# Kernel optimization log

Measured on AMD Instinct MI355X. Metric: run time of the kernel, lower is better.

The kernel has to match this reference:

```python
import math
import jax, jax.numpy as jnp
import numpy as np

HIDDEN = 2048
HEAD_DIM = 128
NUM_HEADS = 32
NUM_KV_HEADS = 8
GROUP = NUM_HEADS // NUM_KV_HEADS
B, S = 1, 2048


def setup_inputs() -> dict:
    key = jax.random.key(0)
    ks = jax.random.split(key, 9)
    scale_in = 1.0 / math.sqrt(HIDDEN)
    scale_o = 1.0 / math.sqrt(NUM_HEADS * HEAD_DIM)
    x = jax.random.normal(ks[0], (B, S, HIDDEN), dtype=jnp.float32)
    # causal mask (1,1,S,S), int32; masked positions are 0
    mask = jnp.tril(jnp.ones((S, S), dtype=jnp.int32))[None, None]
    wq = jax.random.uniform(ks[1], (HIDDEN, NUM_HEADS * HEAD_DIM), jnp.float32, -scale_in, scale_in)
    bq = jax.random.uniform(ks[2], (NUM_HEADS * HEAD_DIM,), jnp.float32, -scale_in, scale_in)
    wk = jax.random.uniform(ks[3], (HIDDEN, NUM_KV_HEADS * HEAD_DIM), jnp.float32, -scale_in, scale_in)
    bk = jax.random.uniform(ks[4], (NUM_KV_HEADS * HEAD_DIM,), jnp.float32, -scale_in, scale_in)
    wv = jax.random.uniform(ks[5], (HIDDEN, NUM_KV_HEADS * HEAD_DIM), jnp.float32, -scale_in, scale_in)
    bv = jax.random.uniform(ks[6], (NUM_KV_HEADS * HEAD_DIM,), jnp.float32, -scale_in, scale_in)
    wo = jax.random.uniform(ks[7], (NUM_HEADS * HEAD_DIM, HIDDEN), jnp.float32, -scale_o, scale_o)
    bo = jax.random.uniform(ks[8], (HIDDEN,), jnp.float32, -scale_o, scale_o)
    return {"x": x, "mask": mask, "wq": wq, "bq": bq, "wk": wk, "bk": bk,
            "wv": wv, "bv": bv, "wo": wo, "bo": bo}


def reference(x, mask, wq, bq, wk, bk, wv, bv, wo, bo):
    Bb, Ss, _ = x.shape
    inv_sqrt_d = 1.0 / math.sqrt(HEAD_DIM)
    # projections
    q = (x @ wq + bq).reshape(Bb, Ss, NUM_KV_HEADS, GROUP, HEAD_DIM)  # grouped query heads
    k = (x @ wk + bk).reshape(Bb, Ss, NUM_KV_HEADS, HEAD_DIM)
    v = (x @ wv + bv).reshape(Bb, Ss, NUM_KV_HEADS, HEAD_DIM)
    # repeat_interleave(group, dim=2) on k/v == broadcasting each kv head over its
    # GROUP consecutive query heads; einsum avoids the physical KV blow-up.
    scores = jnp.einsum('bqhgd,bshd->bhgqs', q, k) * inv_sqrt_d  # (B, Hkv, G, S, S)
    m = mask[:, :, None]  # (1,1,1,S,S) broadcasts over (Hkv, G)
    scores = jnp.where(m == 0, -jnp.inf, scores)
    attn = jax.nn.softmax(scores, axis=-1)
    out = jnp.einsum('bhgqs,bshd->bqhgd', attn, v).reshape(Bb, Ss, NUM_HEADS * HEAD_DIM)
    return out @ wo + bo
```

## Files before the change

kernel.cpp:

```cpp
#include <hip/hip_runtime.h>

#define HIDDEN 2048
#define S_LEN  2048
#define NH     32
#define NKV    8
#define HD     128
#define QKVN   6144
#define OD     4096

typedef float  f32x4   __attribute__((ext_vector_type(4)));
typedef float  f32x16  __attribute__((ext_vector_type(16)));
typedef __bf16 bf16x8  __attribute__((ext_vector_type(8)));
typedef __bf16 bf16x4  __attribute__((ext_vector_type(4)));
typedef unsigned int u32;

static __device__ __forceinline__ f32x4 mfma16(bf16x8 a, bf16x8 b, f32x4 c) {
  return __builtin_amdgcn_mfma_f32_16x16x32_bf16(a, b, c, 0, 0, 0);
}
static __device__ __forceinline__ f32x16 mfma32(bf16x8 a, bf16x8 b, f32x16 c) {
  return __builtin_amdgcn_mfma_f32_32x32x16_bf16(a, b, c, 0, 0, 0);
}
static __device__ __forceinline__ void gload_lds16(const void* g, void* l) {
  __builtin_amdgcn_global_load_lds(
      (__attribute__((address_space(1))) void*)(g),
      (__attribute__((address_space(3))) void*)(l), 16, 0, 0);
}
static __device__ __forceinline__ u32 pk_bf16(float lo, float hi) {
  u32 r;
  asm("v_cvt_pk_bf16_f32 %0, %1, %2" : "=v"(r) : "v"(lo), "v"(hi));
  return r;
}

__global__ __launch_bounds__(256) void k_cvt(const float* __restrict__ in,
                                             __bf16* __restrict__ out, int n) {
  int i = (blockIdx.x * 256 + threadIdx.x) * 4;
  if (i >= n) return;
  float4 v = *reinterpret_cast<const float4*>(in + i);
  bf16x4 o = {(__bf16)v.x, (__bf16)v.y, (__bf16)v.z, (__bf16)v.w};
  *reinterpret_cast<bf16x4*>(out + i) = o;
}

__global__ __launch_bounds__(256) void k_transpose_cvt(const float* __restrict__ src,
                                                       __bf16* __restrict__ dst,
                                                       int K, int N) {
  __shared__ float tile[32][33];
  int tx = threadIdx.x & 31, ty = threadIdx.x >> 5;
  int n0 = blockIdx.x * 32, k0 = blockIdx.y * 32;
#pragma unroll
  for (int r = 0; r < 4; r++) {
    int k = ty + r * 8;
    tile[k][tx] = src[(size_t)(k0 + k) * N + n0 + tx];
  }
  __syncthreads();
#pragma unroll
  for (int r = 0; r < 4; r++) {
    int n = ty + r * 8;
    dst[(size_t)(n0 + n) * K + k0 + tx] = (__bf16)tile[tx][n];
  }
}

__global__ void k_bias_concat(const float* __restrict__ bq, const float* __restrict__ bk,
                              const float* __restrict__ bv, float* __restrict__ out) {
  int i = blockIdx.x * 256 + threadIdx.x;
  if (i >= QKVN) return;
  out[i] = (i < 4096) ? bq[i] : (i < 5120 ? bk[i - 4096] : bv[i - 5120]);
}

__global__ __launch_bounds__(256) void k_vtrans(const __bf16* __restrict__ qkv,
                                                __bf16* __restrict__ vt) {
  __shared__ __bf16 tile[32][33];
  int tx = threadIdx.x & 31, ty = threadIdx.x >> 5;
  int s0 = blockIdx.x * 32, d0 = blockIdx.y * 32, kv = blockIdx.z;
#pragma unroll
  for (int r = 0; r < 4; r++) {
    int s = ty + r * 8;
    tile[s][tx] = qkv[(size_t)(s0 + s) * QKVN + 5120 + kv * HD + d0 + tx];
  }
  __syncthreads();
#pragma unroll
  for (int r = 0; r < 4; r++) {
    int d = ty + r * 8;
    vt[(size_t)(kv * HD + d0 + d) * S_LEN + s0 + tx] = tile[tx][d];
  }
}

__global__ __launch_bounds__(512, 2) void k_gemm8(const __bf16* __restrict__ A,
                                                  const __bf16* __restrict__ BT,
                                                  const float* __restrict__ bias,
                                                  __bf16* __restrict__ C,
                                                  int M, int N, int K,
                                                  float oscale, int scale_cols) {
  __shared__ __bf16 Al[2][2][8192];
  __shared__ __bf16 Bl[2][2][8192];
  const int tid = threadIdx.x, lane = tid & 63, w = tid >> 6;
  const int l15 = lane & 15, lhi = lane >> 4;
  const int wr = w >> 2, wc = w & 3;
  const int mt = blockIdx.x & 7, nt = blockIdx.x >> 3;
  const int m0 = mt * 256, n0 = nt * 256;
  const int NKT = K >> 6;
  const __bf16* Ab = A + (size_t)m0 * K;
  const __bf16* Bb = BT + (size_t)n0 * K;

  f32x4 acc[8][4];
#pragma unroll
  for (int i = 0; i < 8; i++)
#pragma unroll
    for (int j = 0; j < 4; j++)
#pragma unroll
      for (int e = 0; e < 4; e++) acc[i][j][e] = 0.f;

#define SGH(dstA, srcB, buf, kh, ktile)                                           \
  do {                                                                            \
    _Pragma("unroll") for (int it = 0; it < 2; ++it) {                            \
      int c = it * 512 + tid;                                                     \
      int row = c >> 2, slot = c & 3;                                             \
      int scol = ((slot * 16) ^ (((row >> 1) & 3) << 4)) >> 1;                    \
      gload_lds16(srcB + (size_t)row * K + (ktile) * 64 + (kh) * 32 + scol,       \
                  &dstA[buf][kh][c * 8]);                                         \
    }                                                                             \
  } while (0)

#define RD_A(cb, kk)                                                              \
  do {                                                                            \
    _Pragma("unroll") for (int i = 0; i < 8; ++i) {                               \
      int row = wr * 128 + i * 16 + l15;                                          \
      af[i] = *(const bf16x8*)(&Al[cb][kk][row * 32 +                             \
                (((lhi * 16) ^ (((row >> 1) & 3) << 4)) >> 1)]);                  \
    }                                                                             \
  } while (0)

#define RD_B4(cb, kk)                                                             \
  do {                                                                            \
    _Pragma("unroll") for (int j = 0; j < 4; ++j) {                               \
      int row = wc * 64 + j * 16 + l15;                                           \
      bfr[j] = *(const bf16x8*)(&Bl[cb][kk][row * 32 +                            \
                (((lhi * 16) ^ (((row >> 1) & 3) << 4)) >> 1)]);                  \
    }                                                                             \
  } while (0)

#define MFMA32X                                                                   \
  do {                                                                            \
    __builtin_amdgcn_s_setprio(1);                                                \
    _Pragma("unroll") for (int i = 0; i < 8; ++i) {                               \
      _Pragma("unroll") for (int j = 0; j < 4; ++j) {                             \
        acc[i][j] = mfma16(af[i], bfr[j], acc[i][j]);                             \
      }                                                                           \
    }                                                                             \
    __builtin_amdgcn_s_setprio(0);                                                \
  } while (0)

  SGH(Al, Ab, 0, 0, 0);
  SGH(Bl, Bb, 0, 0, 0);
  SGH(Al, Ab, 0, 1, 0);
  SGH(Bl, Bb, 0, 1, 0);
  asm volatile("s_waitcnt vmcnt(4)" ::: "memory");
  __builtin_amdgcn_s_barrier();
  __builtin_amdgcn_sched_barrier(0);

  for (int kt = 0; kt < NKT; ++kt) {
    const int cb = kt & 1, pb = cb ^ 1;
    const bool pf = (kt + 1 < NKT);
    bf16x8 af[8], bfr[4];

    RD_A(cb, 0);
    RD_B4(cb, 0);
    if (pf) { SGH(Al, Ab, pb, 0, kt + 1); SGH(Bl, Bb, pb, 0, kt + 1); }
    __builtin_amdgcn_s_barrier();
    asm volatile("s_waitcnt lgkmcnt(0)" ::: "memory");
    MFMA32X;
    if (pf) {
      asm volatile("s_waitcnt vmcnt(4)" ::: "memory");
    } else {
      asm volatile("s_waitcnt vmcnt(0)" ::: "memory");
    }
    __builtin_amdgcn_s_barrier();
    __builtin_amdgcn_sched_barrier(0);

    RD_A(cb, 1);
    RD_B4(cb, 1);
    if (pf) { SGH(Al, Ab, pb, 1, kt + 1); SGH(Bl, Bb, pb, 1, kt + 1); }
    __builtin_amdgcn_s_barrier();
    asm volatile("s_waitcnt lgkmcnt(0)" ::: "memory");
    MFMA32X;
    if (pf) {
      asm volatile("s_waitcnt vmcnt(4)" ::: "memory");
    }
    __builtin_amdgcn_s_barrier();
    __builtin_amdgcn_sched_barrier(0);
  }
#undef SGH
#undef RD_A
#undef RD_B4
#undef MFMA32X

#pragma unroll
  for (int j = 0; j < 4; j++) {
    int col = n0 + wc * 64 + j * 16 + l15;
    float bv = bias[col];
    float sc = (col < scale_cols) ? oscale : 1.0f;
#pragma unroll
    for (int i = 0; i < 8; i++) {
      int r0 = m0 + wr * 128 + i * 16 + lhi * 4;
#pragma unroll
      for (int rr = 0; rr < 4; rr++) {
        C[(size_t)(r0 + rr) * N + col] = (__bf16)((acc[i][j][rr] + bv) * sc);
      }
    }
  }
}

__global__ __launch_bounds__(256) void k_gemm_part(const __bf16* __restrict__ A,
                                                   const __bf16* __restrict__ BT,
                                                   float* __restrict__ Cpart,
                                                   int M, int N, int K, int KC) {
  __shared__ __bf16 Al[128 * 64];
  __shared__ __bf16 Bl[128 * 64];
  const int tid = threadIdx.x;
  const int lane = tid & 63;
  const int w = tid >> 6;
  const int m0 = blockIdx.y * 128;
  const int n0 = blockIdx.x * 128;
  const int kbeg = blockIdx.z * KC;
  const int wm = (w >> 1) * 64;
  const int wn = (w & 1) * 64;
  const int l15 = lane & 15, lhi = lane >> 4;

  f32x4 acc[4][4];
#pragma unroll
  for (int i = 0; i < 4; i++)
#pragma unroll
    for (int j = 0; j < 4; j++)
#pragma unroll
      for (int e = 0; e < 4; e++) acc[i][j][e] = 0.f;

  for (int kt = kbeg; kt < kbeg + KC; kt += 64) {
#pragma unroll
    for (int it = 0; it < 4; it++) {
      int idx = it * 256 + tid;
      int row = idx >> 3, slot = idx & 7;
      int scol = ((slot * 16) ^ ((row & 7) << 4)) >> 1;
      gload_lds16(A + (size_t)(m0 + row) * K + kt + scol, &Al[idx * 8]);
      gload_lds16(BT + (size_t)(n0 + row) * K + kt + scol, &Bl[idx * 8]);
    }
    __syncthreads();
#pragma unroll
    for (int kk = 0; kk < 2; kk++) {
      bf16x8 af[4], bfr[4];
#pragma unroll
      for (int i = 0; i < 4; i++) {
        int ra = wm + i * 16 + l15;
        int ba = (kk * 64 + lhi * 16) ^ ((ra & 7) << 4);
        af[i] = *(const bf16x8*)((const char*)Al + ra * 128 + ba);
        int rb = wn + i * 16 + l15;
        int bb = (kk * 64 + lhi * 16) ^ ((rb & 7) << 4);
        bfr[i] = *(const bf16x8*)((const char*)Bl + rb * 128 + bb);
      }
#pragma unroll
      for (int i = 0; i < 4; i++)
#pragma unroll
        for (int j = 0; j < 4; j++) acc[i][j] = mfma16(af[i], bfr[j], acc[i][j]);
    }
    __syncthreads();
  }
  float* C = Cpart + (size_t)blockIdx.z * M * N;
#pragma unroll
  for (int j = 0; j < 4; j++) {
    int col = n0 + wn + j * 16 + l15;
#pragma unroll
    for (int i = 0; i < 4; i++) {
      int r0 = m0 + wm + i * 16 + lhi * 4;
#pragma unroll
      for (int rr = 0; rr < 4; rr++) {
        C[(size_t)(r0 + rr) * N + col] = acc[i][j][rr];
      }
    }
  }
}

__global__ __launch_bounds__(256) void k_ocombine(const float* __restrict__ a,
                                                  const float* __restrict__ b,
                                                  const float* __restrict__ bias,
                                                  float* __restrict__ out) {
  int i = (blockIdx.x * 256 + threadIdx.x) * 4;
  f32x4 va = *(const f32x4*)(a + i);
  f32x4 vb = *(const f32x4*)(b + i);
  f32x4 vbias = *(const f32x4*)(bias + (i & (HIDDEN - 1)));
  f32x4 r = va + vb + vbias;
  *(f32x4*)(out + i) = r;
}

__global__ __launch_bounds__(256, 2) void k_attn(const __bf16* __restrict__ qkv,
                                                 const __bf16* __restrict__ vt,
                                                 __bf16* __restrict__ o) {
  __shared__ __bf16 Kl[2][8192];
  __shared__ __bf16 Vl[2][8192];
  const int tid = threadIdx.x, lane = tid & 63, w = tid >> 6;
  const int l31 = lane & 31, h = lane >> 5;

  const int id = blockIdx.x;
  int tile, head;
  if (id < 256) { head = id >> 4; tile = id & 15; }
  else          { head = 16 + ((id - 256) >> 4); tile = 15 - (id & 15); }
  const int kvh = head >> 2;
  const int qbase = tile * 128 + w * 32;
  const int qg = qbase + l31;
  const int kdiag = (qbase + 31) >> 6;
  const int nkt = 2 * tile + 2;

  bf16x8 qf[8];
  {
    const __bf16* qrow = qkv + (size_t)qg * QKVN + head * HD;
#pragma unroll
    for (int dk = 0; dk < 8; dk++) qf[dk] = *(const bf16x8*)(qrow + dk * 16 + h * 8);
  }

  f32x16 acc[4];
#pragma unroll
  for (int dt = 0; dt < 4; dt++)
#pragma unroll
    for (int r = 0; r < 16; r++) acc[dt][r] = 0.f;
  float m = -INFINITY, lsum = 0.f;

#define STAGE(buf, ktile)                                                           \
  do {                                                                              \
    const int kk0 = (ktile) * 64;                                                   \
    _Pragma("unroll") for (int it = 0; it < 4; it++) {                              \
      int c = it * 256 + tid;                                                       \
      int key = c >> 4, slot = c & 15;                                              \
      int scol = ((slot * 16) ^ ((key & 15) << 4)) >> 1;                            \
      gload_lds16(qkv + (size_t)(kk0 + key) * QKVN + 4096 + kvh * HD + scol,        \
                  &Kl[buf][c * 8]);                                                 \
    }                                                                               \
    _Pragma("unroll") for (int it = 0; it < 4; it++) {                              \
      int c = it * 256 + tid;                                                       \
      int d = c >> 3, slot = c & 7;                                                 \
      int scol = ((slot * 16) ^ ((d & 7) << 4)) >> 1;                               \
      gload_lds16(vt + (size_t)(kvh * HD + d) * S_LEN + kk0 + scol,                 \
                  &Vl[buf][c * 8]);                                                 \
    }                                                                               \
  } while (0)

  STAGE(0, 0);
  __syncthreads();

  for (int kt = 0; kt < nkt; kt++) {
    const int cur = kt & 1;
    if (kt + 1 < nkt) STAGE(cur ^ 1, kt + 1);

    if (kt <= kdiag) {
      const char* Kb = (const char*)&Kl[cur][0];
      const char* Vb = (const char*)&Vl[cur][0];
      const int k0 = kt * 64;
      f32x16 sacc[2];
#pragma unroll
      for (int b = 0; b < 2; b++)
#pragma unroll
        for (int r = 0; r < 16; r++) sacc[b][r] = 0.f;
      __builtin_amdgcn_s_setprio(1);
#pragma unroll
      for (int dk = 0; dk < 8; dk++) {
        const int sA = ((2 * dk + h) ^ (l31 & 15)) * 16;
        bf16x8 kf0 = *(const bf16x8*)(Kb + l31 * 256 + sA);
        bf16x8 kf1 = *(const bf16x8*)(Kb + (32 + l31) * 256 + sA);
        sacc[0] = mfma32(kf0, qf[dk], sacc[0]);
        sacc[1] = mfma32(kf1, qf[dk], sacc[1]);
      }
      __builtin_amdgcn_s_setprio(0);
      float p[32];
#pragma unroll
      for (int b = 0; b < 2; b++)
#pragma unroll
        for (int r = 0; r < 16; r++) p[b * 16 + r] = sacc[b][r];
      if (kt == kdiag) {
#pragma unroll
        for (int b = 0; b < 2; b++)
#pragma unroll
          for (int r = 0; r < 16; r++) {
            int keyg = k0 + b * 32 + (r & 3) + 8 * (r >> 2) + 4 * h;
            if (keyg > qg) p[b * 16 + r] = -INFINITY;
          }
      }
      float t16[16], t8[8], t4[4];
#pragma unroll
      for (int i = 0; i < 16; i++) t16[i] = fmaxf(p[2 * i], p[2 * i + 1]);
#pragma unroll
      for (int i = 0; i < 8; i++) t8[i] = fmaxf(t16[2 * i], t16[2 * i + 1]);
#pragma unroll
      for (int i = 0; i < 4; i++) t4[i] = fmaxf(t8[2 * i], t8[2 * i + 1]);
      float pm = fmaxf(fmaxf(t4[0], t4[1]), fmaxf(t4[2], t4[3]));
      pm = fmaxf(pm, __shfl_xor(pm, 32));
      if (__any(pm - m > 8.f)) {
        float mn = fmaxf(m, pm);
        float corr = __expf(m - mn);
        m = mn;
        lsum *= corr;
#pragma unroll
        for (int dt = 0; dt < 4; dt++)
#pragma unroll
          for (int r = 0; r < 16; r++) acc[dt][r] *= corr;
      }
      float psum = 0.f;
#pragma unroll
      for (int i = 0; i < 32; i++) { p[i] = __expf(p[i] - m); psum += p[i]; }
      lsum += psum;
#pragma unroll
      for (int ks2 = 0; ks2 < 4; ks2++) {
        const int o8 = (ks2 >> 1) * 16 + (ks2 & 1) * 8;
        u32 W0 = pk_bf16(p[o8 + 0], p[o8 + 1]);
        u32 W1 = pk_bf16(p[o8 + 2], p[o8 + 3]);
        u32 W2 = pk_bf16(p[o8 + 4], p[o8 + 5]);
        u32 W3 = pk_bf16(p[o8 + 6], p[o8 + 7]);
        asm("v_permlane32_swap_b32 %0, %1" : "+v"(W0), "+v"(W2));
        asm("v_permlane32_swap_b32 %0, %1" : "+v"(W1), "+v"(W3));
        union { u32 wd[4]; bf16x8 v; } pu;
        pu.wd[0] = W0; pu.wd[1] = W1; pu.wd[2] = W2; pu.wd[3] = W3;
        __builtin_amdgcn_s_setprio(1);
#pragma unroll
        for (int dt = 0; dt < 4; dt++) {
          const int dr = dt * 32 + l31;
          const int sV = ((2 * ks2 + h) ^ (dr & 7)) * 16;
          bf16x8 vf = *(const bf16x8*)(Vb + dr * 128 + sV);
          acc[dt] = mfma32(vf, pu.v, acc[dt]);
        }
        __builtin_amdgcn_s_setprio(0);
      }
    }
    __syncthreads();
  }
#undef STAGE

  lsum += __shfl_xor(lsum, 32);
  const float inv = 1.f / lsum;
  __bf16* orow = o + (size_t)qg * OD + head * HD;
#pragma unroll
  for (int dt = 0; dt < 4; dt++)
#pragma unroll
    for (int rq = 0; rq < 4; rq++) {
      int d = dt * 32 + 8 * rq + 4 * h;
      bf16x4 ov = {(__bf16)(acc[dt][rq * 4 + 0] * inv), (__bf16)(acc[dt][rq * 4 + 1] * inv),
                   (__bf16)(acc[dt][rq * 4 + 2] * inv), (__bf16)(acc[dt][rq * 4 + 3] * inv)};
      *(bf16x4*)(orow + d) = ov;
    }
}

extern "C" void kernel_launch(void* const* d_in, const int* in_sizes, int n_in,
                              void* d_out, int out_size, void* d_ws, size_t ws_size,
                              hipStream_t stream) {
  const float* x  = (const float*)d_in[0];
  const float* wq = (const float*)d_in[2];
  const float* bq = (const float*)d_in[3];
  const float* wk = (const float*)d_in[4];
  const float* bk = (const float*)d_in[5];
  const float* wv = (const float*)d_in[6];
  const float* bv = (const float*)d_in[7];
  const float* wo = (const float*)d_in[8];
  const float* bo = (const float*)d_in[9];
  float* out = (float*)d_out;

  const size_t MB = 1024 * 1024;
  char* ws = (char*)d_ws;
  __bf16* xb    = (__bf16*)(ws);
  __bf16* wqkvT = (__bf16*)(ws + 8 * MB);
  __bf16* woT   = (__bf16*)(ws + 32 * MB);
  __bf16* qkvb  = (__bf16*)(ws + 48 * MB);
  __bf16* vtb   = (__bf16*)(ws + 72 * MB);
  __bf16* ob    = (__bf16*)(ws + 76 * MB);
  float*  bqkv  = (float*)(ws + 92 * MB);
  float*  Cpart = (float*)(ws);

  k_cvt<<<4096, 256, 0, stream>>>(x, xb, HIDDEN * S_LEN);
  k_transpose_cvt<<<dim3(128, 64), 256, 0, stream>>>(wq, wqkvT, HIDDEN, 4096);
  k_transpose_cvt<<<dim3(32, 64), 256, 0, stream>>>(wk, wqkvT + (size_t)4096 * HIDDEN, HIDDEN, 1024);
  k_transpose_cvt<<<dim3(32, 64), 256, 0, stream>>>(wv, wqkvT + (size_t)5120 * HIDDEN, HIDDEN, 1024);
  k_transpose_cvt<<<dim3(64, 128), 256, 0, stream>>>(wo, woT, 4096, HIDDEN);
  k_bias_concat<<<24, 256, 0, stream>>>(bq, bk, bv, bqkv);

  k_gemm8<<<192, 512, 0, stream>>>(xb, wqkvT, bqkv, qkvb, S_LEN, QKVN, HIDDEN,
                                   0.08838834764831845f, 4096);
  k_vtrans<<<dim3(S_LEN / 32, HD / 32, NKV), 256, 0, stream>>>(qkvb, vtb);
  k_attn<<<512, 256, 0, stream>>>(qkvb, vtb, ob);
  k_gemm_part<<<dim3(HIDDEN / 128, S_LEN / 128, 2), 256, 0, stream>>>(
      ob, woT, Cpart, S_LEN, HIDDEN, OD, OD / 2);
  k_ocombine<<<(S_LEN * HIDDEN) / 1024, 256, 0, stream>>>(
      Cpart, Cpart + (size_t)S_LEN * HIDDEN, bo, out);
}
```

Before: 224.6 us.

## Retile QKV GEMM to 128x192 tiles with 256 threads and XCD-aware block swizzle

The QKV projection GEMM moves from 192 blocks of 256x256 tiles with 512 threads to 512 blocks of 128x192 tiles with 256 threads. Each wave now covers all 128 rows and a 48-column slice, and the load and wait counts change to match. A block index swizzle groups tiles per XCD so neighbouring blocks share operands in cache. The aim is to fill all 256 CUs (192 blocks left many idle) at the cost of lower per-tile data reuse and more redundant global loads.

```diff
diff --git a/kernel.cpp b/kernel.cpp
--- a/kernel.cpp
+++ b/kernel.cpp
@@ -84,123 +84,121 @@
   }
 }
 
-__global__ __launch_bounds__(512, 2) void k_gemm8(const __bf16* __restrict__ A,
+__global__ __launch_bounds__(256, 2) void k_gemm8(const __bf16* __restrict__ A,
                                                   const __bf16* __restrict__ BT,
                                                   const float* __restrict__ bias,
                                                   __bf16* __restrict__ C,
                                                   int M, int N, int K,
                                                   float oscale, int scale_cols) {
-  __shared__ __bf16 Al[2][2][8192];
-  __shared__ __bf16 Bl[2][2][8192];
+  __shared__ __bf16 Al[2][2][4096];
+  __shared__ __bf16 Bl[2][2][6144];
   const int tid = threadIdx.x, lane = tid & 63, w = tid >> 6;
   const int l15 = lane & 15, lhi = lane >> 4;
-  const int wr = w >> 2, wc = w & 3;
-  const int mt = blockIdx.x & 7, nt = blockIdx.x >> 3;
-  const int m0 = mt * 256, n0 = nt * 256;
+  const int sw = ((blockIdx.x & 7) << 6) + (blockIdx.x >> 3);
+  const int mt = sw & 15, nt = sw >> 4;
+  const int m0 = mt * 128, n0 = nt * 192;
   const int NKT = K >> 6;
   const __bf16* Ab = A + (size_t)m0 * K;
   const __bf16* Bb = BT + (size_t)n0 * K;
 
-  f32x4 acc[8][4];
+  f32x4 acc[8][3];
 #pragma unroll
   for (int i = 0; i < 8; i++)
 #pragma unroll
-    for (int j = 0; j < 4; j++)
+    for (int j = 0; j < 3; j++)
 #pragma unroll
       for (int e = 0; e < 4; e++) acc[i][j][e] = 0.f;
 
-#define SGH(dstA, srcB, buf, kh, ktile)                                           \
+#define SGH(buf, kh, ktile)                                                       \
   do {                                                                            \
     _Pragma("unroll") for (int it = 0; it < 2; ++it) {                            \
-      int c = it * 512 + tid;                                                     \
+      int c = it * 256 + tid;                                                     \
       int row = c >> 2, slot = c & 3;                                             \
       int scol = ((slot * 16) ^ (((row >> 1) & 3) << 4)) >> 1;                    \
-      gload_lds16(srcB + (size_t)row * K + (ktile) * 64 + (kh) * 32 + scol,       \
-                  &dstA[buf][kh][c * 8]);                                         \
+      gload_lds16(Ab + (size_t)row * K + (ktile) * 64 + (kh) * 32 + scol,         \
+                  &Al[buf][kh][c * 8]);                                           \
+    }                                                                             \
+    _Pragma("unroll") for (int it = 0; it < 3; ++it) {                            \
+      int c = it * 256 + tid;                                                     \
+      int row = c >> 2, slot = c & 3;                                             \
+      int scol = ((slot * 16) ^ (((row >> 1) & 3) << 4)) >> 1;                    \
+      gload_lds16(Bb + (size_t)row * K + (ktile) * 64 + (kh) * 32 + scol,         \
+                  &Bl[buf][kh][c * 8]);                                           \
     }                                                                             \
   } while (0)
 
-#define RD_A(cb, kk)                                                              \
+#define RD_AB(cb, kk)                                                             \
   do {                                                                            \
     _Pragma("unroll") for (int i = 0; i < 8; ++i) {                               \
-      int row = wr * 128 + i * 16 + l15;                                          \
+      int row = i * 16 + l15;                                                     \
       af[i] = *(const bf16x8*)(&Al[cb][kk][row * 32 +                             \
                 (((lhi * 16) ^ (((row >> 1) & 3) << 4)) >> 1)]);                  \
     }                                                                             \
-  } while (0)
-
-#define RD_B4(cb, kk)                                                             \
-  do {                                                                            \
-    _Pragma("unroll") for (int j = 0; j < 4; ++j) {                               \
-      int row = wc * 64 + j * 16 + l15;                                           \
+    _Pragma("unroll") for (int j = 0; j < 3; ++j) {                               \
+      int row = w * 48 + j * 16 + l15;                                            \
       bfr[j] = *(const bf16x8*)(&Bl[cb][kk][row * 32 +                            \
                 (((lhi * 16) ^ (((row >> 1) & 3) << 4)) >> 1)]);                  \
     }                                                                             \
   } while (0)
 
-#define MFMA32X                                                                   \
+#define MFMA24X                                                                   \
   do {                                                                            \
     __builtin_amdgcn_s_setprio(1);                                                \
     _Pragma("unroll") for (int i = 0; i < 8; ++i) {                               \
-      _Pragma("unroll") for (int j = 0; j < 4; ++j) {                             \
+      _Pragma("unroll") for (int j = 0; j < 3; ++j) {                             \
         acc[i][j] = mfma16(af[i], bfr[j], acc[i][j]);                             \
       }                                                                           \
     }                                                                             \
     __builtin_amdgcn_s_setprio(0);                                                \
   } while (0)
 
-  SGH(Al, Ab, 0, 0, 0);
-  SGH(Bl, Bb, 0, 0, 0);
-  SGH(Al, Ab, 0, 1, 0);
-  SGH(Bl, Bb, 0, 1, 0);
-  asm volatile("s_waitcnt vmcnt(4)" ::: "memory");
+  SGH(0, 0, 0);
+  SGH(0, 1, 0);
+  asm volatile("s_waitcnt vmcnt(5)" ::: "memory");
   __builtin_amdgcn_s_barrier();
   __builtin_amdgcn_sched_barrier(0);
 
   for (int kt = 0; kt < NKT; ++kt) {
     const int cb = kt & 1, pb = cb ^ 1;
     const bool pf = (kt + 1 < NKT);
-    bf16x8 af[8], bfr[4];
-
-    RD_A(cb, 0);
-    RD_B4(cb, 0);
-    if (pf) { SGH(Al, Ab, pb, 0, kt + 1); SGH(Bl, Bb, pb, 0, kt + 1); }
+    bf16x8 af[8], bfr[3];
+
+    RD_AB(cb, 0);
+    if (pf) SGH(pb, 0, kt + 1);
     __builtin_amdgcn_s_barrier();
     asm volatile("s_waitcnt lgkmcnt(0)" ::: "memory");
-    MFMA32X;
+    MFMA24X;
     if (pf) {
-      asm volatile("s_waitcnt vmcnt(4)" ::: "memory");
+      asm volatile("s_waitcnt vmcnt(5)" ::: "memory");
     } else {
       asm volatile("s_waitcnt vmcnt(0)" ::: "memory");
     }
     __builtin_amdgcn_s_barrier();
     __builtin_amdgcn_sched_barrier(0);
 
-    RD_A(cb, 1);
-    RD_B4(cb, 1);
-    if (pf) { SGH(Al, Ab, pb, 1, kt + 1); SGH(Bl, Bb, pb, 1, kt + 1); }
+    RD_AB(cb, 1);
+    if (pf) SGH(pb, 1, kt + 1);
     __builtin_amdgcn_s_barrier();
     asm volatile("s_waitcnt lgkmcnt(0)" ::: "memory");
-    MFMA32X;
+    MFMA24X;
     if (pf) {
-      asm volatile("s_waitcnt vmcnt(4)" ::: "memory");
+      asm volatile("s_waitcnt vmcnt(5)" ::: "memory");
     }
     __builtin_amdgcn_s_barrier();
     __builtin_amdgcn_sched_barrier(0);
   }
 #undef SGH
-#undef RD_A
-#undef RD_B4
-#undef MFMA32X
-
-#pragma unroll
-  for (int j = 0; j < 4; j++) {
-    int col = n0 + wc * 64 + j * 16 + l15;
+#undef RD_AB
+#undef MFMA24X
+
+#pragma unroll
+  for (int j = 0; j < 3; j++) {
+    int col = n0 + w * 48 + j * 16 + l15;
     float bv = bias[col];
     float sc = (col < scale_cols) ? oscale : 1.0f;
 #pragma unroll
     for (int i = 0; i < 8; i++) {
-      int r0 = m0 + wr * 128 + i * 16 + lhi * 4;
+      int r0 = m0 + i * 16 + lhi * 4;
 #pragma unroll
       for (int rr = 0; rr < 4; rr++) {
         C[(size_t)(r0 + rr) * N + col] = (__bf16)((acc[i][j][rr] + bv) * sc);
@@ -475,7 +473,7 @@
   k_transpose_cvt<<<dim3(64, 128), 256, 0, stream>>>(wo, woT, 4096, HIDDEN);
   k_bias_concat<<<24, 256, 0, stream>>>(bq, bk, bv, bqkv);
 
-  k_gemm8<<<192, 512, 0, stream>>>(xb, wqkvT, bqkv, qkvb, S_LEN, QKVN, HIDDEN,
+  k_gemm8<<<512, 256, 0, stream>>>(xb, wqkvT, bqkv, qkvb, S_LEN, QKVN, HIDDEN,
                                    0.08838834764831845f, 4096);
   k_vtrans<<<dim3(S_LEN / 32, HD / 32, NKV), 256, 0, stream>>>(qkvb, vtb);
   k_attn<<<512, 256, 0, stream>>>(qkvb, vtb, ob);
```

Measured after the change: 218.3 us. -2.8%, faster.
